# Performance work log

Hardware: AMD Instinct MI355X
Metric: run time of the kernel (lower is better)

## Reference

```python
import jax, jax.numpy as jnp
import numpy as np

T, H, I, E, TOP_K = 4096, 2048, 768, 16, 2


def _pack_i2s(tern):
    # tern: int8 in {-1,0,1}, shape [..., K] with K % 4 == 0
    m = (tern + 1).astype(jnp.uint8)  # map to {0,1,2}
    m = m.reshape(*tern.shape[:-1], -1, 4)
    return (m[..., 0] | (m[..., 1] << 2) | (m[..., 2] << 4) | (m[..., 3] << 6)).astype(jnp.uint8)


def _quantize_alpha(alpha):
    # per-column alpha -> int8 with global scale (quantize_alpha_int8)
    scale = jnp.maximum(jnp.abs(alpha).max(), 1e-8) / 127.0
    q = jnp.clip(jnp.round(alpha / scale), -128, 127).astype(jnp.int8)
    return q, scale.astype(jnp.float32)


def _unpack_i2s(packed, K, alpha):
    # packed: uint8 [..., N, K//4]; alpha: [..., K] per input column
    shifts = jnp.array([0, 2, 4, 6], dtype=jnp.uint8)
    ext = (packed[..., None] >> shifts) & jnp.uint8(3)  # [..., N, K//4, 4]
    vals = ext.reshape(*packed.shape[:-1], K).astype(jnp.float32) - 1.0  # {-1,0,1}
    return vals * alpha[..., None, :]


def setup_inputs() -> dict:
    key = jax.random.key(0)
    ks = jax.random.split(key, 6)
    x = jax.random.normal(ks[0], (T, H), dtype=jnp.float32)
    router_logits = jax.random.normal(ks[1], (T, E), dtype=jnp.float32)
    tern13 = jax.random.randint(ks[2], (E, 2 * I, H), -1, 2, dtype=jnp.int8)
    tern2 = jax.random.randint(ks[3], (E, H, I), -1, 2, dtype=jnp.int8)
    a13 = jax.random.uniform(ks[4], (E, H), minval=0.01, maxval=0.05, dtype=jnp.float32)
    a2 = jax.random.uniform(ks[5], (E, I), minval=0.01, maxval=0.05, dtype=jnp.float32)
    w13_alpha_q, w13_alpha_scale = _quantize_alpha(a13)
    w2_alpha_q, w2_alpha_scale = _quantize_alpha(a2)
    return {
        "x": x,
        "router_logits": router_logits,
        "w13_packed": _pack_i2s(tern13),
        "w13_alpha_q": w13_alpha_q,
        "w13_alpha_scale": w13_alpha_scale,
        "w2_packed": _pack_i2s(tern2),
        "w2_alpha_q": w2_alpha_q,
        "w2_alpha_scale": w2_alpha_scale,
    }


def reference(x, router_logits, w13_packed, w13_alpha_q, w13_alpha_scale,
              w2_packed, w2_alpha_q, w2_alpha_scale):
    # dequant int8 alphas, then dequant 2-bit ternary weights
    a13 = w13_alpha_q.astype(jnp.float32) * w13_alpha_scale  # [E, H]
    a2 = w2_alpha_q.astype(jnp.float32) * w2_alpha_scale     # [E, I]
    w13 = _unpack_i2s(w13_packed, H, a13)  # [E, 2I, H]
    w2 = _unpack_i2s(w2_packed, I, a2)     # [E, H, I]

    # top-k routing with renormalized softmax weights
    probs = jax.nn.softmax(router_logits, axis=-1)
    topw, topi = jax.lax.top_k(probs, TOP_K)           # [T, k]
    topw = topw / topw.sum(axis=-1, keepdims=True)
    combine = jnp.sum(jax.nn.one_hot(topi, E, dtype=x.dtype) * topw[..., None], axis=1)  # [T, E]

    # grouped expert matmuls (dense dispatch over experts)
    gu = jnp.einsum('th,enh->ten', x, w13)             # [T, E, 2I]
    gate, up = jnp.split(gu, 2, axis=-1)
    act = jax.nn.silu(gate) * up                       # [T, E, I]
    down = jnp.einsum('tei,ehi->teh', act, w2)         # [T, E, H]
    return jnp.einsum('te,teh->th', combine, down)     # [T, H]
```

## Files before the change

### kernel.cpp

```cpp
#include <hip/hip_runtime.h>
#include <stdint.h>

#define T_TOK 4096
#define HDIM  2048
#define IDIM  768
#define NEXP  16
#define NPAIR (T_TOK * 2)
#define PAIR_CAP (NPAIR + 256)

typedef float f32x4 __attribute__((ext_vector_type(4)));
typedef __bf16 bf16x8 __attribute__((ext_vector_type(8)));
typedef unsigned short u16x8 __attribute__((ext_vector_type(8)));
typedef unsigned int u32;
typedef const __attribute__((address_space(1))) u32* as1_u32p;
typedef __attribute__((address_space(3))) u32* as3_u32p;

__device__ __forceinline__ unsigned short f2bf(float f) {
  u32 u = __float_as_uint(f);
  u += 0x7FFFu + ((u >> 16) & 1u);
  return (unsigned short)(u >> 16);
}

__device__ __forceinline__ unsigned short tb(int m) {
  return m == 0 ? (unsigned short)0xBF80 : (m == 2 ? (unsigned short)0x3F80 : (unsigned short)0);
}

__device__ __forceinline__ f32x4 mfma16(bf16x8 a, bf16x8 b, f32x4 c) {
  return __builtin_amdgcn_mfma_f32_16x16x32_bf16(a, b, c, 0, 0, 0);
}

__global__ __launch_bounds__(256) void route_kernel(
    const float* __restrict__ logits, int* __restrict__ counts,
    int* __restrict__ t2i, float* __restrict__ t2w) {
  const int t = blockIdx.x * 256 + threadIdx.x;
  if (t >= T_TOK) return;
  const float* l = logits + t * NEXP;
  float m0 = -1e30f, m1 = -1e30f;
  int i0 = 0, i1 = 0;
#pragma unroll
  for (int j = 0; j < NEXP; ++j) {
    const float v = l[j];
    if (v > m0) { m1 = m0; i1 = i0; m0 = v; i0 = j; }
    else if (v > m1) { m1 = v; i1 = j; }
  }
  const float w0 = 1.0f / (1.0f + expf(m1 - m0));
  t2i[t] = i0 | (i1 << 8);
  t2w[t] = w0;
  atomicAdd(&counts[i0], 1);
  atomicAdd(&counts[i1], 1);
}

__global__ void scan_kernel(const int* __restrict__ counts,
                            int* __restrict__ offs, int* __restrict__ cursor) {
  if (threadIdx.x == 0) {
    int s = 0;
    for (int e = 0; e < NEXP; ++e) { offs[e] = s; cursor[e] = s; s += counts[e]; }
    offs[NEXP] = s;
  }
}

__global__ __launch_bounds__(256) void fill_kernel(
    const int* __restrict__ t2i, const float* __restrict__ t2w,
    int* __restrict__ cursor, int* __restrict__ pair_token,
    float* __restrict__ pair_wt, int* __restrict__ pair_eid,
    int* __restrict__ t2p0, int* __restrict__ t2p1) {
  const int t = blockIdx.x * 256 + threadIdx.x;
  if (t >= T_TOK) return;
  const int ii = t2i[t];
  const float w0 = t2w[t];
  const int i0 = ii & 255, i1 = (ii >> 8) & 255;
  const int p0 = atomicAdd(&cursor[i0], 1);
  pair_token[p0] = t; pair_wt[p0] = w0; pair_eid[p0] = i0;
  const int p1 = atomicAdd(&cursor[i1], 1);
  pair_token[p1] = t; pair_wt[p1] = 1.0f - w0; pair_eid[p1] = i1;
  t2p0[t] = p0; t2p1[t] = p1;
}

__global__ __launch_bounds__(256) void repack_kernel(
    const int* __restrict__ w, u32* __restrict__ o) {
  const int j0 = (blockIdx.x * 256 + threadIdx.x) * 4;
  const int4* w4 = (const int4*)w;
  uint4 r;
#pragma unroll
  for (int k = 0; k < 4; ++k) {
    const int4 a = w4[j0 + k];
    ((u32*)&r)[k] = (u32)(a.x & 255) | ((u32)(a.y & 255) << 8) |
                    ((u32)(a.z & 255) << 16) | ((u32)(a.w & 255) << 24);
  }
  ((uint4*)o)[blockIdx.x * 256 + threadIdx.x] = r;
}

__global__ __launch_bounds__(256) void xg_kernel(
    const float* __restrict__ x, const int* __restrict__ a13q,
    const float* __restrict__ s13p, const int* __restrict__ pair_token,
    const int* __restrict__ pair_eid, unsigned short* __restrict__ xg) {
  const int p = blockIdx.x;
  const int t = pair_token[p];
  const int e = pair_eid[p];
  const float s13 = *s13p;
  const int h0 = threadIdx.x * 8;
  const float* xp = x + (size_t)t * HDIM + h0;
  const int* ap = a13q + (size_t)e * HDIM + h0;
  const float4 x0 = ((const float4*)xp)[0];
  const float4 x1 = ((const float4*)xp)[1];
  const int4 a0 = ((const int4*)ap)[0];
  const int4 a1 = ((const int4*)ap)[1];
  u16x8 q;
  q[0] = f2bf(x0.x * (float)a0.x * s13);
  q[1] = f2bf(x0.y * (float)a0.y * s13);
  q[2] = f2bf(x0.z * (float)a0.z * s13);
  q[3] = f2bf(x0.w * (float)a0.w * s13);
  q[4] = f2bf(x1.x * (float)a1.x * s13);
  q[5] = f2bf(x1.y * (float)a1.y * s13);
  q[6] = f2bf(x1.z * (float)a1.z * s13);
  q[7] = f2bf(x1.w * (float)a1.w * s13);
  *(u16x8*)(xg + (size_t)p * HDIM + h0) = q;
}

#define STAGE_B(sBx, wb)                                                   \
  {                                                                        \
    unsigned short* dst = sBx + sBoff;                                     \
    const uint2 q0 = lut[(wb) & 255], q1 = lut[((wb) >> 8) & 255];         \
    const uint2 q2 = lut[((wb) >> 16) & 255], q3 = lut[(wb) >> 24];        \
    *(uint2*)(dst + 0) = q0;                                               \
    *(uint2*)(dst + 4) = q1;                                               \
    *(uint2*)(dst + 8) = q2;                                               \
    *(uint2*)(dst + 12) = q3;                                              \
  }

__global__ __launch_bounds__(256, 4) void gemm1_kernel(
    const u32* __restrict__ wq13, const int* __restrict__ a2q,
    const float* __restrict__ s2p, const int* __restrict__ counts,
    const int* __restrict__ offs, const float* __restrict__ pair_wt,
    const unsigned short* __restrict__ xg, unsigned short* __restrict__ act) {
  const int id = blockIdx.x;
  const int xcd = id & 7, sblk = id >> 3;
  const int nT = sblk % 12;
  const int gg = (sblk / 12) * 8 + xcd;
  const int e = gg & 15, mT = gg >> 4;
  const int cnt = counts[e];
  if (mT * 128 >= cnt) return;
  const int base = offs[e];
  const int tid = threadIdx.x;

  __shared__ unsigned short sA0[128 * 32];
  __shared__ unsigned short sA1[128 * 32];
  __shared__ unsigned short sB0[128 * 36 + 8];
  __shared__ unsigned short sB1[128 * 36 + 8];
  __shared__ uint2 lut[256];

  {
    const int b = tid;
    const u32 lo = (u32)tb(b & 3) | ((u32)tb((b >> 2) & 3) << 16);
    const u32 hi = (u32)tb((b >> 4) & 3) | ((u32)tb((b >> 6) & 3) << 16);
    lut[b] = make_uint2(lo, hi);
  }
  __syncthreads();

  const int wave = tid >> 6, lane = tid & 63;
  const int wm = wave >> 1, wn = wave & 1;
  const int quad = lane >> 4, ln = lane & 15;

  const int bn = tid >> 1, bhalf = tid & 1;
  const int grow = (bn < 64) ? (nT * 64 + bn) : (IDIM + nT * 64 + (bn - 64));
  const u32* browp = wq13 + ((size_t)e * (2 * IDIM) + grow) * (HDIM / 16);
  const int sBoff = bn * 36 + (bhalf << 4);

  const int arow = lane >> 2;
  const int acol = (lane & 3) * 8;
  const size_t arow0 = (size_t)(base + mT * 128);

  f32x4 acc[4][4] = {};

#define G1_MFMA(sAx, sBx)                                                          \
  {                                                                                \
    bf16x8 af[4];                                                                  \
    _Pragma("unroll") for (int mi = 0; mi < 4; ++mi)                               \
        af[mi] = *(const bf16x8*)(sAx + (wm * 64 + mi * 16 + ln) * 32 + quad * 8); \
    bf16x8 b0 = *(const bf16x8*)(sBx + (wn * 32 + ln) * 36 + quad * 8);            \
    bf16x8 b1 = *(const bf16x8*)(sBx + (wn * 32 + 16 + ln) * 36 + quad * 8);       \
    bf16x8 b2 = *(const bf16x8*)(sBx + (64 + wn * 32 + ln) * 36 + quad * 8);       \
    bf16x8 b3 = *(const bf16x8*)(sBx + (64 + wn * 32 + 16 + ln) * 36 + quad * 8);  \
    _Pragma("unroll") for (int mi = 0; mi < 4; ++mi) {                             \
      acc[mi][0] = mfma16(af[mi], b0, acc[mi][0]);                                 \
      acc[mi][1] = mfma16(af[mi], b1, acc[mi][1]);                                 \
      acc[mi][2] = mfma16(af[mi], b2, acc[mi][2]);                                 \
      acc[mi][3] = mfma16(af[mi], b3, acc[mi][3]);                                 \
    }                                                                              \
  }

  for (int s = 0; s < HDIM / 64; ++s) {
    const uint4 W = *(const uint4*)(browp + 4 * s);
#pragma unroll
    for (int c = 0; c < 2; ++c) {
      const unsigned short* gp =
          xg + (arow0 + wave * 32 + c * 16 + arow) * HDIM + s * 64 + acol;
      unsigned short* lp = sA0 + (wave * 32 + c * 16) * 32;
      __builtin_amdgcn_global_load_lds((as1_u32p)(const void*)gp, (as3_u32p)(void*)lp, 16, 0, 0);
    }
#pragma unroll
    for (int c = 0; c < 2; ++c) {
      const unsigned short* gp =
          xg + (arow0 + wave * 32 + c * 16 + arow) * HDIM + s * 64 + 32 + acol;
      unsigned short* lp = sA1 + (wave * 32 + c * 16) * 32;
      __builtin_amdgcn_global_load_lds((as1_u32p)(const void*)gp, (as3_u32p)(void*)lp, 16, 0, 0);
    }
    {
      const u32 wlo = bhalf ? W.y : W.x;
      const u32 whi = bhalf ? W.w : W.z;
      STAGE_B(sB0, wlo);
      STAGE_B(sB1, whi);
    }
    __syncthreads();
    G1_MFMA(sA0, sB0);
    G1_MFMA(sA1, sB1);
    __syncthreads();
  }

  const float s2 = *s2p;
#pragma unroll
  for (int gi = 0; gi < 2; ++gi) {
    const int i = nT * 64 + wn * 32 + gi * 16 + ln;
    const float a2v = (float)a2q[e * IDIM + i] * s2;
#pragma unroll
    for (int mi = 0; mi < 4; ++mi) {
      const f32x4 g = acc[mi][gi];
      const f32x4 u = acc[mi][gi + 2];
#pragma unroll
      for (int r = 0; r < 4; ++r) {
        const int m = mT * 128 + wm * 64 + mi * 16 + quad * 4 + r;
        if (m < cnt) {
          const float wt = pair_wt[base + m];
          const float gv = g[r];
          const float av = gv / (1.0f + __expf(-gv)) * u[r] * a2v * wt;
          act[(size_t)(base + m) * IDIM + i] = f2bf(av);
        }
      }
    }
  }
}

__global__ __launch_bounds__(256, 4) void gemm2_kernel(
    const u32* __restrict__ wq2, const int* __restrict__ counts,
    const int* __restrict__ offs, const unsigned short* __restrict__ act,
    unsigned short* __restrict__ down) {
  const int id = blockIdx.x;
  const int xcd = id & 7, sblk = id >> 3;
  const int nT = sblk & 15;
  const int gg = (sblk >> 4) * 8 + xcd;
  const int e = gg & 15, mT = gg >> 4;
  const int cnt = counts[e];
  if (mT * 128 >= cnt) return;
  const int base = offs[e];
  const int tid = threadIdx.x;

  __shared__ unsigned short sA0[128 * 32];
  __shared__ unsigned short sA1[128 * 32];
  __shared__ unsigned short sB0[128 * 36 + 8];
  __shared__ unsigned short sB1[128 * 36 + 8];
  __shared__ uint2 lut[256];

  {
    const int b = tid;
    const u32 lo = (u32)tb(b & 3) | ((u32)tb((b >> 2) & 3) << 16);
    const u32 hi = (u32)tb((b >> 4) & 3) | ((u32)tb((b >> 6) & 3) << 16);
    lut[b] = make_uint2(lo, hi);
  }
  __syncthreads();

  const int wave = tid >> 6, lane = tid & 63;
  const int wm = wave >> 1, wn = wave & 1;
  const int quad = lane >> 4, ln = lane & 15;

  const int bn = tid >> 1, bhalf = tid & 1;
  const u32* browp = wq2 + ((size_t)e * HDIM + nT * 128 + bn) * (IDIM / 16);
  const int sBoff = bn * 36 + (bhalf << 4);

  const int arow = lane >> 2;
  const int acol = (lane & 3) * 8;
  const size_t arow0 = (size_t)(base + mT * 128);

  f32x4 acc[4][4] = {};

#define G2_MFMA(sAx, sBx)                                                          \
  {                                                                                \
    bf16x8 af[4];                                                                  \
    _Pragma("unroll") for (int mi = 0; mi < 4; ++mi)                               \
        af[mi] = *(const bf16x8*)(sAx + (wm * 64 + mi * 16 + ln) * 32 + quad * 8); \
    bf16x8 b0 = *(const bf16x8*)(sBx + (wn * 64 + ln) * 36 + quad * 8);            \
    bf16x8 b1 = *(const bf16x8*)(sBx + (wn * 64 + 16 + ln) * 36 + quad * 8);       \
    bf16x8 b2 = *(const bf16x8*)(sBx + (wn * 64 + 32 + ln) * 36 + quad * 8);       \
    bf16x8 b3 = *(const bf16x8*)(sBx + (wn * 64 + 48 + ln) * 36 + quad * 8);       \
    _Pragma("unroll") for (int mi = 0; mi < 4; ++mi) {                             \
      acc[mi][0] = mfma16(af[mi], b0, acc[mi][0]);                                 \
      acc[mi][1] = mfma16(af[mi], b1, acc[mi][1]);                                 \
      acc[mi][2] = mfma16(af[mi], b2, acc[mi][2]);                                 \
      acc[mi][3] = mfma16(af[mi], b3, acc[mi][3]);                                 \
    }                                                                              \
  }

  for (int s = 0; s < IDIM / 64; ++s) {
    const uint4 W = *(const uint4*)(browp + 4 * s);
#pragma unroll
    for (int c = 0; c < 2; ++c) {
      const unsigned short* gp =
          act + (arow0 + wave * 32 + c * 16 + arow) * IDIM + s * 64 + acol;
      unsigned short* lp = sA0 + (wave * 32 + c * 16) * 32;
      __builtin_amdgcn_global_load_lds((as1_u32p)(const void*)gp, (as3_u32p)(void*)lp, 16, 0, 0);
    }
#pragma unroll
    for (int c = 0; c < 2; ++c) {
      const unsigned short* gp =
          act + (arow0 + wave * 32 + c * 16 + arow) * IDIM + s * 64 + 32 + acol;
      unsigned short* lp = sA1 + (wave * 32 + c * 16) * 32;
      __builtin_amdgcn_global_load_lds((as1_u32p)(const void*)gp, (as3_u32p)(void*)lp, 16, 0, 0);
    }
    {
      const u32 wlo = bhalf ? W.y : W.x;
      const u32 whi = bhalf ? W.w : W.z;
      STAGE_B(sB0, wlo);
      STAGE_B(sB1, whi);
    }
    __syncthreads();
    G2_MFMA(sA0, sB0);
    G2_MFMA(sA1, sB1);
    __syncthreads();
  }

#pragma unroll
  for (int mi = 0; mi < 4; ++mi) {
#pragma unroll
    for (int r = 0; r < 4; ++r) {
      const int ml = wm * 64 + mi * 16 + quad * 4 + r;
      const int m = mT * 128 + ml;
      if (m < cnt) {
        unsigned short* drow = down + (size_t)(base + m) * HDIM + nT * 128 + wn * 64;
#pragma unroll
        for (int ni = 0; ni < 4; ++ni)
          drow[ni * 16 + ln] = f2bf(acc[mi][ni][r]);
      }
    }
  }
}

__global__ __launch_bounds__(256) void combine_kernel(
    const int* __restrict__ t2p0, const int* __restrict__ t2p1,
    const unsigned short* __restrict__ down, float* __restrict__ out) {
  const int t = blockIdx.x;
  const int h = threadIdx.x * 8;
  const u16x8 a = *(const u16x8*)(down + (size_t)t2p0[t] * HDIM + h);
  const u16x8 b = *(const u16x8*)(down + (size_t)t2p1[t] * HDIM + h);
  f32x4 o0, o1;
#pragma unroll
  for (int j = 0; j < 4; ++j) {
    o0[j] = __uint_as_float((u32)a[j] << 16) + __uint_as_float((u32)b[j] << 16);
    o1[j] = __uint_as_float((u32)a[j + 4] << 16) + __uint_as_float((u32)b[j + 4] << 16);
  }
  float* o = out + (size_t)t * HDIM + h;
  *(f32x4*)(o) = o0;
  *(f32x4*)(o + 4) = o1;
}

extern "C" void kernel_launch(void* const* d_in, const int* in_sizes, int n_in,
                              void* d_out, int out_size, void* d_ws, size_t ws_size,
                              hipStream_t stream) {
  const float* x      = (const float*)d_in[0];
  const float* logits = (const float*)d_in[1];
  const int*   w13p   = (const int*)d_in[2];
  const int*   a13q   = (const int*)d_in[3];
  const float* s13    = (const float*)d_in[4];
  const int*   w2p    = (const int*)d_in[5];
  const int*   a2q    = (const int*)d_in[6];
  const float* s2     = (const float*)d_in[7];
  float* out = (float*)d_out;

  char* ws = (char*)d_ws;
  int*   counts     = (int*)(ws + 0);
  int*   cursor     = (int*)(ws + 64);
  int*   offs       = (int*)(ws + 128);
  int*   t2i        = (int*)(ws + 256);
  float* t2w        = (float*)(ws + 256 + 4 * T_TOK);
  int*   t2p0       = (int*)(ws + 256 + 8 * T_TOK);
  int*   t2p1       = (int*)(ws + 256 + 12 * T_TOK);
  int*   pair_token = (int*)(ws + 256 + 16 * T_TOK);
  float* pair_wt    = (float*)(ws + 256 + 16 * T_TOK + 4 * PAIR_CAP);
  int*   pair_eid   = (int*)(ws + 256 + 16 * T_TOK + 8 * PAIR_CAP);
  const size_t hdr_end = ((size_t)(256 + 16 * T_TOK + 12 * PAIR_CAP) + 255) & ~(size_t)255;

  const size_t n32_13 = (size_t)NEXP * 2 * IDIM * (HDIM / 16);
  const size_t n32_2  = (size_t)NEXP * HDIM * (IDIM / 16);
  const size_t rp13_b = n32_13 * 4, rp2_b = n32_2 * 4;
  const size_t xg_b   = (size_t)PAIR_CAP * HDIM * 2;

  u32* rp13 = (u32*)(ws + hdr_end);
  u32* rp2  = (u32*)(ws + hdr_end + rp13_b);
  unsigned short* xg  = (unsigned short*)(ws + hdr_end + rp13_b + rp2_b);
  unsigned short* act = (unsigned short*)(ws + hdr_end + rp13_b + rp2_b + xg_b);
  unsigned short* down = xg;

  hipMemsetAsync(counts, 0, 256, stream);
  route_kernel<<<T_TOK / 256, 256, 0, stream>>>(logits, counts, t2i, t2w);
  scan_kernel<<<1, 64, 0, stream>>>(counts, offs, cursor);
  fill_kernel<<<T_TOK / 256, 256, 0, stream>>>(t2i, t2w, cursor, pair_token, pair_wt,
                                               pair_eid, t2p0, t2p1);
  repack_kernel<<<(int)(n32_13 / 1024), 256, 0, stream>>>(w13p, rp13);
  repack_kernel<<<(int)(n32_2 / 1024), 256, 0, stream>>>(w2p, rp2);
  xg_kernel<<<NPAIR, 256, 0, stream>>>(x, a13q, s13, pair_token, pair_eid, xg);

  gemm1_kernel<<<6144, 256, 0, stream>>>(rp13, a2q, s2, counts, offs, pair_wt, xg, act);
  gemm2_kernel<<<8192, 256, 0, stream>>>(rp2, counts, offs, act, down);
  combine_kernel<<<T_TOK, 256, 0, stream>>>(t2p0, t2p1, down, out);
}
```

Before: 347.4 us.

## Replace LUT ternary decode with byte-permute decode and prefetch next weight tile

Removes the shared-memory lookup table from both grouped GEMM kernels. Ternary weights are now decoded in registers with v_perm byte shuffles, and the repack kernel pre-shuffles the packed bits to fit that layout. The next step's packed weight word is register-prefetched so its global latency overlaps the current step's MFMA work. The LDS B-tile row stride grows from 36 to 40 for 16-byte aligned vector stores. This trades LDS gathers and the LUT setup barrier for a few ALU ops, at the cost of a bit more register pressure and LDS.

```diff
diff --git a/kernel.cpp b/kernel.cpp
--- a/kernel.cpp
+++ b/kernel.cpp
@@ -21,12 +21,22 @@
   return (unsigned short)(u >> 16);
 }
 
-__device__ __forceinline__ unsigned short tb(int m) {
-  return m == 0 ? (unsigned short)0xBF80 : (m == 2 ? (unsigned short)0x3F80 : (unsigned short)0);
-}
-
 __device__ __forceinline__ f32x4 mfma16(bf16x8 a, bf16x8 b, f32x4 c) {
   return __builtin_amdgcn_mfma_f32_16x16x32_bf16(a, b, c, 0, 0, 0);
+}
+
+__device__ __forceinline__ void stage16(unsigned short* dst, u32 w) {
+  u32 o[8];
+#pragma unroll
+  for (int i = 0; i < 4; ++i) {
+    const u32 t  = (w >> (2 * i)) & 0x03030303u;
+    const u32 hb = __builtin_amdgcn_perm(0u, 0x003F00BFu, t);
+    const u32 lb = __builtin_amdgcn_perm(0u, 0x00800080u, t);
+    o[2 * i]     = __builtin_amdgcn_perm(hb, lb, 0x05010400u);
+    o[2 * i + 1] = __builtin_amdgcn_perm(hb, lb, 0x07030602u);
+  }
+  *(uint4*)(dst + 0) = make_uint4(o[0], o[1], o[2], o[3]);
+  *(uint4*)(dst + 8) = make_uint4(o[4], o[5], o[6], o[7]);
 }
 
 __global__ __launch_bounds__(256) void route_kernel(
@@ -84,8 +94,11 @@
 #pragma unroll
   for (int k = 0; k < 4; ++k) {
     const int4 a = w4[j0 + k];
-    ((u32*)&r)[k] = (u32)(a.x & 255) | ((u32)(a.y & 255) << 8) |
-                    ((u32)(a.z & 255) << 16) | ((u32)(a.w & 255) << 24);
+    u32 x = (u32)(a.x & 255) | ((u32)(a.y & 255) << 8) |
+            ((u32)(a.z & 255) << 16) | ((u32)(a.w & 255) << 24);
+    u32 t = (x ^ (x >> 12)) & 0x0000F0F0u; x ^= t ^ (t << 12);
+    t = (x ^ (x >> 6)) & 0x00CC00CCu;      x ^= t ^ (t << 6);
+    ((u32*)&r)[k] = x;
   }
   ((uint4*)o)[blockIdx.x * 256 + threadIdx.x] = r;
 }
@@ -117,17 +130,6 @@
   *(u16x8*)(xg + (size_t)p * HDIM + h0) = q;
 }
 
-#define STAGE_B(sBx, wb)                                                   \
-  {                                                                        \
-    unsigned short* dst = sBx + sBoff;                                     \
-    const uint2 q0 = lut[(wb) & 255], q1 = lut[((wb) >> 8) & 255];         \
-    const uint2 q2 = lut[((wb) >> 16) & 255], q3 = lut[(wb) >> 24];        \
-    *(uint2*)(dst + 0) = q0;                                               \
-    *(uint2*)(dst + 4) = q1;                                               \
-    *(uint2*)(dst + 8) = q2;                                               \
-    *(uint2*)(dst + 12) = q3;                                              \
-  }
-
 __global__ __launch_bounds__(256, 4) void gemm1_kernel(
     const u32* __restrict__ wq13, const int* __restrict__ a2q,
     const float* __restrict__ s2p, const int* __restrict__ counts,
@@ -143,19 +145,10 @@
   const int base = offs[e];
   const int tid = threadIdx.x;
 
-  __shared__ unsigned short sA0[128 * 32];
-  __shared__ unsigned short sA1[128 * 32];
-  __shared__ unsigned short sB0[128 * 36 + 8];
-  __shared__ unsigned short sB1[128 * 36 + 8];
-  __shared__ uint2 lut[256];
-
-  {
-    const int b = tid;
-    const u32 lo = (u32)tb(b & 3) | ((u32)tb((b >> 2) & 3) << 16);
-    const u32 hi = (u32)tb((b >> 4) & 3) | ((u32)tb((b >> 6) & 3) << 16);
-    lut[b] = make_uint2(lo, hi);
-  }
-  __syncthreads();
+  __shared__ __align__(16) unsigned short sA0[128 * 32];
+  __shared__ __align__(16) unsigned short sA1[128 * 32];
+  __shared__ __align__(16) unsigned short sB0[128 * 40];
+  __shared__ __align__(16) unsigned short sB1[128 * 40];
 
   const int wave = tid >> 6, lane = tid & 63;
   const int wm = wave >> 1, wn = wave & 1;
@@ -164,7 +157,7 @@
   const int bn = tid >> 1, bhalf = tid & 1;
   const int grow = (bn < 64) ? (nT * 64 + bn) : (IDIM + nT * 64 + (bn - 64));
   const u32* browp = wq13 + ((size_t)e * (2 * IDIM) + grow) * (HDIM / 16);
-  const int sBoff = bn * 36 + (bhalf << 4);
+  const int sBoff = bn * 40 + (bhalf << 4);
 
   const int arow = lane >> 2;
   const int acol = (lane & 3) * 8;
@@ -177,10 +170,10 @@
     bf16x8 af[4];                                                                  \
     _Pragma("unroll") for (int mi = 0; mi < 4; ++mi)                               \
         af[mi] = *(const bf16x8*)(sAx + (wm * 64 + mi * 16 + ln) * 32 + quad * 8); \
-    bf16x8 b0 = *(const bf16x8*)(sBx + (wn * 32 + ln) * 36 + quad * 8);            \
-    bf16x8 b1 = *(const bf16x8*)(sBx + (wn * 32 + 16 + ln) * 36 + quad * 8);       \
-    bf16x8 b2 = *(const bf16x8*)(sBx + (64 + wn * 32 + ln) * 36 + quad * 8);       \
-    bf16x8 b3 = *(const bf16x8*)(sBx + (64 + wn * 32 + 16 + ln) * 36 + quad * 8);  \
+    bf16x8 b0 = *(const bf16x8*)(sBx + (wn * 32 + ln) * 40 + quad * 8);            \
+    bf16x8 b1 = *(const bf16x8*)(sBx + (wn * 32 + 16 + ln) * 40 + quad * 8);       \
+    bf16x8 b2 = *(const bf16x8*)(sBx + (64 + wn * 32 + ln) * 40 + quad * 8);       \
+    bf16x8 b3 = *(const bf16x8*)(sBx + (64 + wn * 32 + 16 + ln) * 40 + quad * 8);  \
     _Pragma("unroll") for (int mi = 0; mi < 4; ++mi) {                             \
       acc[mi][0] = mfma16(af[mi], b0, acc[mi][0]);                                 \
       acc[mi][1] = mfma16(af[mi], b1, acc[mi][1]);                                 \
@@ -189,8 +182,8 @@
     }                                                                              \
   }
 
+  uint4 W = *(const uint4*)(browp);
   for (int s = 0; s < HDIM / 64; ++s) {
-    const uint4 W = *(const uint4*)(browp + 4 * s);
 #pragma unroll
     for (int c = 0; c < 2; ++c) {
       const unsigned short* gp =
@@ -205,16 +198,15 @@
       unsigned short* lp = sA1 + (wave * 32 + c * 16) * 32;
       __builtin_amdgcn_global_load_lds((as1_u32p)(const void*)gp, (as3_u32p)(void*)lp, 16, 0, 0);
     }
-    {
-      const u32 wlo = bhalf ? W.y : W.x;
-      const u32 whi = bhalf ? W.w : W.z;
-      STAGE_B(sB0, wlo);
-      STAGE_B(sB1, whi);
-    }
+    const int sn = (s + 1 < HDIM / 64) ? s + 1 : s;
+    const uint4 Wn = *(const uint4*)(browp + 4 * sn);
+    stage16(sB0 + sBoff, bhalf ? W.y : W.x);
+    stage16(sB1 + sBoff, bhalf ? W.w : W.z);
     __syncthreads();
     G1_MFMA(sA0, sB0);
     G1_MFMA(sA1, sB1);
     __syncthreads();
+    W = Wn;
   }
 
   const float s2 = *s2p;
@@ -254,19 +246,10 @@
   const int base = offs[e];
   const int tid = threadIdx.x;
 
-  __shared__ unsigned short sA0[128 * 32];
-  __shared__ unsigned short sA1[128 * 32];
-  __shared__ unsigned short sB0[128 * 36 + 8];
-  __shared__ unsigned short sB1[128 * 36 + 8];
-  __shared__ uint2 lut[256];
-
-  {
-    const int b = tid;
-    const u32 lo = (u32)tb(b & 3) | ((u32)tb((b >> 2) & 3) << 16);
-    const u32 hi = (u32)tb((b >> 4) & 3) | ((u32)tb((b >> 6) & 3) << 16);
-    lut[b] = make_uint2(lo, hi);
-  }
-  __syncthreads();
+  __shared__ __align__(16) unsigned short sA0[128 * 32];
+  __shared__ __align__(16) unsigned short sA1[128 * 32];
+  __shared__ __align__(16) unsigned short sB0[128 * 40];
+  __shared__ __align__(16) unsigned short sB1[128 * 40];
 
   const int wave = tid >> 6, lane = tid & 63;
   const int wm = wave >> 1, wn = wave & 1;
@@ -274,7 +257,7 @@
 
   const int bn = tid >> 1, bhalf = tid & 1;
   const u32* browp = wq2 + ((size_t)e * HDIM + nT * 128 + bn) * (IDIM / 16);
-  const int sBoff = bn * 36 + (bhalf << 4);
+  const int sBoff = bn * 40 + (bhalf << 4);
 
   const int arow = lane >> 2;
   const int acol = (lane & 3) * 8;
@@ -287,10 +270,10 @@
     bf16x8 af[4];                                                                  \
     _Pragma("unroll") for (int mi = 0; mi < 4; ++mi)                               \
         af[mi] = *(const bf16x8*)(sAx + (wm * 64 + mi * 16 + ln) * 32 + quad * 8); \
-    bf16x8 b0 = *(const bf16x8*)(sBx + (wn * 64 + ln) * 36 + quad * 8);            \
-    bf16x8 b1 = *(const bf16x8*)(sBx + (wn * 64 + 16 + ln) * 36 + quad * 8);       \
-    bf16x8 b2 = *(const bf16x8*)(sBx + (wn * 64 + 32 + ln) * 36 + quad * 8);       \
-    bf16x8 b3 = *(const bf16x8*)(sBx + (wn * 64 + 48 + ln) * 36 + quad * 8);       \
+    bf16x8 b0 = *(const bf16x8*)(sBx + (wn * 64 + ln) * 40 + quad * 8);            \
+    bf16x8 b1 = *(const bf16x8*)(sBx + (wn * 64 + 16 + ln) * 40 + quad * 8);       \
+    bf16x8 b2 = *(const bf16x8*)(sBx + (wn * 64 + 32 + ln) * 40 + quad * 8);       \
+    bf16x8 b3 = *(const bf16x8*)(sBx + (wn * 64 + 48 + ln) * 40 + quad * 8);       \
     _Pragma("unroll") for (int mi = 0; mi < 4; ++mi) {                             \
       acc[mi][0] = mfma16(af[mi], b0, acc[mi][0]);                                 \
       acc[mi][1] = mfma16(af[mi], b1, acc[mi][1]);                                 \
@@ -299,8 +282,8 @@
     }                                                                              \
   }
 
+  uint4 W = *(const uint4*)(browp);
   for (int s = 0; s < IDIM / 64; ++s) {
-    const uint4 W = *(const uint4*)(browp + 4 * s);
 #pragma unroll
     for (int c = 0; c < 2; ++c) {
       const unsigned short* gp =
@@ -315,16 +298,15 @@
       unsigned short* lp = sA1 + (wave * 32 + c * 16) * 32;
       __builtin_amdgcn_global_load_lds((as1_u32p)(const void*)gp, (as3_u32p)(void*)lp, 16, 0, 0);
     }
-    {
-      const u32 wlo = bhalf ? W.y : W.x;
-      const u32 whi = bhalf ? W.w : W.z;
-      STAGE_B(sB0, wlo);
-      STAGE_B(sB1, whi);
-    }
+    const int sn = (s + 1 < IDIM / 64) ? s + 1 : s;
+    const uint4 Wn = *(const uint4*)(browp + 4 * sn);
+    stage16(sB0 + sBoff, bhalf ? W.y : W.x);
+    stage16(sB1 + sBoff, bhalf ? W.w : W.z);
     __syncthreads();
     G2_MFMA(sA0, sB0);
     G2_MFMA(sA1, sB1);
     __syncthreads();
+    W = Wn;
   }
 
 #pragma unroll
```

After: 335.6 us. 3.4% less time.
